# Performance work log

Measured on AMD Instinct MI355X. Metric: run time of the kernel, lower is better.

The kernel has to match this reference:

```python
import jax, jax.numpy as jnp
import numpy as np

DIM = 512
N_DAYS = 24

def setup_inputs() -> dict:
    key = jax.random.key(0)
    k1, k2, k3, k4 = jax.random.split(key, 4)
    x = jax.random.normal(k1, (64, 1024, DIM), dtype=jnp.float32)
    day_ids = jax.random.randint(k2, (64,), 0, N_DAYS, dtype=jnp.int64)
    W = jax.random.normal(k3, (N_DAYS, DIM, DIM), dtype=jnp.float32) * 0.02 + jnp.eye(DIM, dtype=jnp.float32)
    b = jax.random.normal(k4, (N_DAYS, DIM), dtype=jnp.float32) * 0.02
    return {"x": x, "day_ids": day_ids, "W": W, "b": b}

def reference(x, day_ids, W, b):
    # Gather per-sample day weights/biases, batched matmul + bias, softsign.
    # (Dropout is identity in eval mode.)
    Wd = W[day_ids]            # [B, dim, dim]
    bd = b[day_ids][:, None, :]  # [B, 1, dim]
    y = jnp.einsum('btd,bde->bte', x, Wd) + bd
    return y / (1.0 + jnp.abs(y))  # Softsign
```

## Files before the change

kernel.cpp:

```cpp
#include <hip/hip_runtime.h>


#define DIM 512
#define SEQ 1024
#define NB 64
#define NDAYS 24
#define BM 128
#define BN 128
#define BK 64
#define LDA (BK + 8)

typedef __bf16 bf16x8 __attribute__((ext_vector_type(8)));
typedef __bf16 bf16x4 __attribute__((ext_vector_type(4)));
typedef float  f32x4  __attribute__((ext_vector_type(4)));

__device__ __forceinline__ void gll16(const void* g, void* l) {
    __builtin_amdgcn_global_load_lds(
        (const __attribute__((address_space(1))) unsigned int*)g,
        (__attribute__((address_space(3))) unsigned int*)l,
        16, 0, 0);
}

__global__ __launch_bounds__(256)
void transpose_w_kernel(const float* __restrict__ W, __bf16* __restrict__ Wt) {
    __shared__ __bf16 T[32][33];
    const int d  = blockIdx.z;
    const int k0 = blockIdx.x * 32;
    const int n0 = blockIdx.y * 32;
    const int tx = threadIdx.x & 31;
    const int ty = threadIdx.x >> 5;
    const float* Wd = W + (size_t)d * DIM * DIM;
    #pragma unroll
    for (int i = 0; i < 4; ++i) {
        const int k = ty + i * 8;
        T[tx][k] = (__bf16)Wd[(size_t)(k0 + k) * DIM + n0 + tx];
    }
    __syncthreads();
    __bf16* Wtd = Wt + (size_t)d * DIM * DIM;
    #pragma unroll
    for (int i = 0; i < 4; ++i) {
        const int n = ty + i * 8;
        Wtd[(size_t)(n0 + n) * DIM + k0 + tx] = T[n][tx];
    }
}

__global__ __launch_bounds__(256, 4)
void day_adapter_kernel(const float* __restrict__ x,
                        const int*   __restrict__ day_ids,
                        const __bf16* __restrict__ Wt,
                        const float* __restrict__ bias,
                        float*       __restrict__ out)
{
    __shared__ __align__(16) __bf16 As[BM][LDA];
    __shared__ __align__(16) __bf16 Bs[BN * BK];

    const int L  = blockIdx.x;
    const int g  = (L >> 3) & 3;
    const int mb = (L & 7) | ((L >> 5) << 3);
    const int m  = mb & 7;
    const int bb = mb >> 3;

    const int n0  = g * BN;
    const int m0  = m * BM;
    const int tid = threadIdx.x;
    const int day = day_ids[bb];

    const float*  xb  = x   + (size_t)bb  * SEQ * DIM + (size_t)m0 * DIM;
    const __bf16* Wtb = Wt  + (size_t)day * DIM * DIM + (size_t)n0 * DIM;
    float*        ob  = out + (size_t)bb  * SEQ * DIM + (size_t)m0 * DIM + n0;

    const int wave = tid >> 6;
    const int lane = tid & 63;
    const int wm   = (wave >> 1) * 64;
    const int wn   = (wave & 1) * 64;
    const int l15  = lane & 15;
    const int quad = lane >> 4;
    const int kq   = quad * 8;

    const int a_row = tid >> 2;
    const int a_col = (tid & 3) * 4;

    char* BsB = (char*)Bs;

    f32x4 acc[4][4];
    const f32x4 zero = {0.f, 0.f, 0.f, 0.f};
    #pragma unroll
    for (int i = 0; i < 4; ++i)
        #pragma unroll
        for (int j = 0; j < 4; ++j) acc[i][j] = zero;

    for (int kk = 0; kk < DIM; kk += BK) {
        #pragma unroll
        for (int p = 0; p < 4; ++p) {
            const int s  = p * 256 + tid;
            const int n  = s >> 3;
            const int cp = s & 7;
            const int c  = cp ^ (n & 7);
            gll16(Wtb + (size_t)n * DIM + kk + c * 8,
                  BsB + (size_t)(p * 256 + (tid & ~63)) * 16);
        }
        #pragma unroll
        for (int h = 0; h < 2; ++h) {
            const int r = a_row + h * 64;
            #pragma unroll
            for (int i = 0; i < 4; ++i) {
                const int col = a_col + i * 16;
                const float4 f = *(const float4*)(xb + (size_t)r * DIM + kk + col);
                bf16x4 v;
                v[0] = (__bf16)f.x; v[1] = (__bf16)f.y;
                v[2] = (__bf16)f.z; v[3] = (__bf16)f.w;
                *(bf16x4*)&As[r][col] = v;
            }
        }
        __syncthreads();

        #pragma unroll
        for (int ks = 0; ks < 2; ++ks) {
            bf16x8 af[4], bfr[4];
            #pragma unroll
            for (int i = 0; i < 4; ++i)
                af[i] = *(const bf16x8*)&As[wm + i * 16 + l15][ks * 32 + kq];
            #pragma unroll
            for (int j = 0; j < 4; ++j) {
                const int n  = wn + j * 16 + l15;
                const int c  = ks * 4 + quad;
                const int cp = c ^ (n & 7);
                bfr[j] = *(const bf16x8*)&Bs[n * BK + cp * 8];
            }
            #pragma unroll
            for (int i = 0; i < 4; ++i)
                #pragma unroll
                for (int j = 0; j < 4; ++j)
                    acc[i][j] = __builtin_amdgcn_mfma_f32_16x16x32_bf16(
                        af[i], bfr[j], acc[i][j], 0, 0, 0);
        }
        __syncthreads();
    }

    float bv[4];
    #pragma unroll
    for (int j = 0; j < 4; ++j)
        bv[j] = bias[(size_t)day * DIM + n0 + wn + j * 16 + l15];

    #pragma unroll
    for (int i = 0; i < 4; ++i) {
        const int rbase = wm + i * 16 + quad * 4;
        #pragma unroll
        for (int j = 0; j < 4; ++j) {
            const int col = wn + j * 16 + l15;
            #pragma unroll
            for (int r = 0; r < 4; ++r) {
                const float y = acc[i][j][r] + bv[j];
                ob[(size_t)(rbase + r) * DIM + col] = y / (1.0f + fabsf(y));
            }
        }
    }
}

extern "C" void kernel_launch(void* const* d_in, const int* in_sizes, int n_in,
                              void* d_out, int out_size, void* d_ws, size_t ws_size,
                              hipStream_t stream) {
    const float* x       = (const float*)d_in[0];
    const int*   day_ids = (const int*)  d_in[1];
    const float* W       = (const float*)d_in[2];
    const float* bias    = (const float*)d_in[3];
    float*       out     = (float*)d_out;
    __bf16*      Wt      = (__bf16*)d_ws;

    dim3 tgrid(DIM / 32, DIM / 32, NDAYS);
    transpose_w_kernel<<<tgrid, 256, 0, stream>>>(W, Wt);

    day_adapter_kernel<<<dim3(2048), 256, 0, stream>>>(x, day_ids, Wt, bias, out);
}
```

Before: 279.2 us.

## Double-buffer LDS tiles, prefetch x into registers, use 512-thread blocks

The GEMM main loop now double-buffers both the A (x) and B (Wt) tiles in LDS. Global loads for the next K step are issued right after one barrier, so they overlap with the MFMA work on the current buffer, and the second barrier per iteration is removed. The block grows to 8 waves, each computing a 64x32 sub-tile, and the A tile switches from padding to an XOR swizzle. LDS use doubles to 64KB per block, which may limit occupancy against the launch bound of 4.

After: 293.3 us. 1.05x slower.

```diff
diff --git a/kernel.cpp b/kernel.cpp
--- a/kernel.cpp
+++ b/kernel.cpp
@@ -3,15 +3,13 @@
 
 #define DIM 512
 #define SEQ 1024
-#define NB 64
 #define NDAYS 24
 #define BM 128
 #define BN 128
 #define BK 64
-#define LDA (BK + 8)
+#define NITER (DIM / BK)
 
 typedef __bf16 bf16x8 __attribute__((ext_vector_type(8)));
-typedef __bf16 bf16x4 __attribute__((ext_vector_type(4)));
 typedef float  f32x4  __attribute__((ext_vector_type(4)));
 
 __device__ __forceinline__ void gll16(const void* g, void* l) {
@@ -44,15 +42,15 @@
     }
 }
 
-__global__ __launch_bounds__(256, 4)
+__global__ __launch_bounds__(512, 4)
 void day_adapter_kernel(const float* __restrict__ x,
                         const int*   __restrict__ day_ids,
                         const __bf16* __restrict__ Wt,
                         const float* __restrict__ bias,
                         float*       __restrict__ out)
 {
-    __shared__ __align__(16) __bf16 As[BM][LDA];
-    __shared__ __align__(16) __bf16 Bs[BN * BK];
+    __shared__ __align__(16) __bf16 As[2][BM * BK];
+    __shared__ __align__(16) __bf16 Bs[2][BN * BK];
 
     const int L  = blockIdx.x;
     const int g  = (L >> 3) & 3;
@@ -71,82 +69,104 @@
 
     const int wave = tid >> 6;
     const int lane = tid & 63;
-    const int wm   = (wave >> 1) * 64;
-    const int wn   = (wave & 1) * 64;
+    const int wm   = (wave & 1) * 64;
+    const int wn   = (wave >> 1) * 32;
     const int l15  = lane & 15;
     const int quad = lane >> 4;
-    const int kq   = quad * 8;
 
-    const int a_row = tid >> 2;
-    const int a_col = (tid & 3) * 4;
+    const int ar  = tid >> 2;
+    const int acg = tid & 3;
 
-    char* BsB = (char*)Bs;
-
-    f32x4 acc[4][4];
+    f32x4 acc[4][2];
     const f32x4 zero = {0.f, 0.f, 0.f, 0.f};
     #pragma unroll
-    for (int i = 0; i < 4; ++i)
-        #pragma unroll
-        for (int j = 0; j < 4; ++j) acc[i][j] = zero;
+    for (int i = 0; i < 4; ++i) { acc[i][0] = zero; acc[i][1] = zero; }
 
-    for (int kk = 0; kk < DIM; kk += BK) {
-        #pragma unroll
-        for (int p = 0; p < 4; ++p) {
-            const int s  = p * 256 + tid;
-            const int n  = s >> 3;
-            const int cp = s & 7;
-            const int c  = cp ^ (n & 7);
-            gll16(Wtb + (size_t)n * DIM + kk + c * 8,
-                  BsB + (size_t)(p * 256 + (tid & ~63)) * 16);
+    float4 areg[4];
+
+    #pragma unroll
+    for (int p = 0; p < 2; ++p) {
+        const int s = p * 512 + tid;
+        const int n = s >> 3;
+        const int c = (s & 7) ^ (n & 7);
+        gll16(Wtb + (size_t)n * DIM + c * 8,
+              (char*)Bs[0] + (size_t)(p * 512 + (tid & ~63)) * 16);
+    }
+    #pragma unroll
+    for (int p = 0; p < 4; ++p)
+        areg[p] = *(const float4*)(xb + (size_t)ar * DIM + acg * 16 + p * 4);
+
+    for (int it = 0; it < NITER; ++it) {
+        const int cur = it & 1;
+        const int nxt = cur ^ 1;
+
+        {
+            bf16x8 w0, w1;
+            w0[0] = (__bf16)areg[0].x; w0[1] = (__bf16)areg[0].y;
+            w0[2] = (__bf16)areg[0].z; w0[3] = (__bf16)areg[0].w;
+            w0[4] = (__bf16)areg[1].x; w0[5] = (__bf16)areg[1].y;
+            w0[6] = (__bf16)areg[1].z; w0[7] = (__bf16)areg[1].w;
+            w1[0] = (__bf16)areg[2].x; w1[1] = (__bf16)areg[2].y;
+            w1[2] = (__bf16)areg[2].z; w1[3] = (__bf16)areg[2].w;
+            w1[4] = (__bf16)areg[3].x; w1[5] = (__bf16)areg[3].y;
+            w1[6] = (__bf16)areg[3].z; w1[7] = (__bf16)areg[3].w;
+            const int c0 = (2 * acg)     ^ (ar & 7);
+            const int c1 = (2 * acg + 1) ^ (ar & 7);
+            *(bf16x8*)&As[cur][ar * BK + c0 * 8] = w0;
+            *(bf16x8*)&As[cur][ar * BK + c1 * 8] = w1;
         }
-        #pragma unroll
-        for (int h = 0; h < 2; ++h) {
-            const int r = a_row + h * 64;
+
+        __syncthreads();
+
+        if (it + 1 < NITER) {
+            const int kk = (it + 1) * BK;
             #pragma unroll
-            for (int i = 0; i < 4; ++i) {
-                const int col = a_col + i * 16;
-                const float4 f = *(const float4*)(xb + (size_t)r * DIM + kk + col);
-                bf16x4 v;
-                v[0] = (__bf16)f.x; v[1] = (__bf16)f.y;
-                v[2] = (__bf16)f.z; v[3] = (__bf16)f.w;
-                *(bf16x4*)&As[r][col] = v;
+            for (int p = 0; p < 2; ++p) {
+                const int s = p * 512 + tid;
+                const int n = s >> 3;
+                const int c = (s & 7) ^ (n & 7);
+                gll16(Wtb + (size_t)n * DIM + kk + c * 8,
+                      (char*)Bs[nxt] + (size_t)(p * 512 + (tid & ~63)) * 16);
             }
+            #pragma unroll
+            for (int p = 0; p < 4; ++p)
+                areg[p] = *(const float4*)(xb + (size_t)ar * DIM + kk + acg * 16 + p * 4);
         }
-        __syncthreads();
 
         #pragma unroll
         for (int ks = 0; ks < 2; ++ks) {
-            bf16x8 af[4], bfr[4];
+            bf16x8 af[4], bfr[2];
             #pragma unroll
-            for (int i = 0; i < 4; ++i)
-                af[i] = *(const bf16x8*)&As[wm + i * 16 + l15][ks * 32 + kq];
+            for (int i = 0; i < 4; ++i) {
+                const int mr = wm + i * 16 + l15;
+                const int c  = (ks * 4 + quad) ^ (mr & 7);
+                af[i] = *(const bf16x8*)&As[cur][mr * BK + c * 8];
+            }
             #pragma unroll
-            for (int j = 0; j < 4; ++j) {
-                const int n  = wn + j * 16 + l15;
-                const int c  = ks * 4 + quad;
-                const int cp = c ^ (n & 7);
-                bfr[j] = *(const bf16x8*)&Bs[n * BK + cp * 8];
+            for (int j = 0; j < 2; ++j) {
+                const int nr = wn + j * 16 + l15;
+                const int c  = (ks * 4 + quad) ^ (nr & 7);
+                bfr[j] = *(const bf16x8*)&Bs[cur][nr * BK + c * 8];
             }
             #pragma unroll
             for (int i = 0; i < 4; ++i)
                 #pragma unroll
-                for (int j = 0; j < 4; ++j)
+                for (int j = 0; j < 2; ++j)
                     acc[i][j] = __builtin_amdgcn_mfma_f32_16x16x32_bf16(
                         af[i], bfr[j], acc[i][j], 0, 0, 0);
         }
-        __syncthreads();
     }
 
-    float bv[4];
+    float bv[2];
     #pragma unroll
-    for (int j = 0; j < 4; ++j)
+    for (int j = 0; j < 2; ++j)
         bv[j] = bias[(size_t)day * DIM + n0 + wn + j * 16 + l15];
 
     #pragma unroll
     for (int i = 0; i < 4; ++i) {
         const int rbase = wm + i * 16 + quad * 4;
         #pragma unroll
-        for (int j = 0; j < 4; ++j) {
+        for (int j = 0; j < 2; ++j) {
             const int col = wn + j * 16 + l15;
             #pragma unroll
             for (int r = 0; r < 4; ++r) {
@@ -170,5 +190,5 @@
     dim3 tgrid(DIM / 32, DIM / 32, NDAYS);
     transpose_w_kernel<<<tgrid, 256, 0, stream>>>(W, Wt);
 
-    day_adapter_kernel<<<dim3(2048), 256, 0, stream>>>(x, day_ids, Wt, bias, out);
+    day_adapter_kernel<<<dim3(2048), 512, 0, stream>>>(x, day_ids, Wt, bias, out);
 }
```
